# Kernel optimization log

Hardware: AMD Instinct MI355X
Metric: run time of the kernel (lower is better)

## Reference

```python
import jax, jax.numpy as jnp
import numpy as np

B, T, D = 4, 4096, 1024
EPS = 1e-5


def _layernorm(x, w):
    mu = jnp.mean(x, axis=-1, keepdims=True)
    var = jnp.var(x, axis=-1, keepdims=True)
    return (x - mu) * jax.lax.rsqrt(var + EPS) * w


def setup_inputs() -> dict:
    key = jax.random.key(0)
    k0, k1, k2, k3 = jax.random.split(key, 4)
    x = jax.random.normal(k0, (B, T, D), dtype=jnp.float32)
    lengths = jax.random.randint(k1, (B,), 1, T + 1, dtype=jnp.int32)
    ln1_w = jnp.ones((D,), dtype=jnp.float32)
    ln2_w = jnp.ones((D,), dtype=jnp.float32)
    Wfc = jax.random.normal(k2, (D, 4 * D), dtype=jnp.float32) * 0.02
    Wproj = jax.random.normal(k3, (4 * D, D), dtype=jnp.float32) * 0.02
    return {"x": x, "lengths": lengths, "ln1_w": ln1_w, "ln2_w": ln2_w,
            "Wfc": Wfc, "Wproj": Wproj}


def reference(x, lengths, ln1_w, ln2_w, Wfc, Wproj):
    b, t, d = x.shape
    # valid[b, i] = i < lengths[b]  (non-padded positions)
    valid = (jnp.arange(t)[None, :] < lengths[:, None]).astype(x.dtype)  # (B,T)

    # --- FusedQueryAtt: out[b,i] = h[b,i] + valid_i * sum_{j<=i} valid_j * gelu(h[b,j])
    h = _layernorm(x, ln1_w)
    g = jax.nn.gelu(h, approximate=False) * valid[:, :, None]  # (B,T,D)
    attn_out = h + valid[:, :, None] * jnp.cumsum(g, axis=1)
    x = x + attn_out  # residual around attn

    # --- MLP (bias=False, dropout=0 in eval)
    h2 = _layernorm(x, ln2_w)
    mlp_out = jax.nn.gelu(h2 @ Wfc, approximate=False) @ Wproj
    return x + mlp_out
```

## Files before the change

kernel.cpp:

```cpp
#include <hip/hip_runtime.h>
#include <hip/hip_bf16.h>
#include <math.h>

#define B_SZ 4
#define T_SZ 4096
#define D_SZ 1024
#define H_SZ 4096
#define CHUNK 16
#define NCHUNK (T_SZ / CHUNK)
#define LN_EPS 1e-5f

using frag8 = __attribute__((ext_vector_type(8))) short;
using f32x4 = __attribute__((ext_vector_type(4))) float;

__device__ __forceinline__ float gelu_exact(float x) {
  return 0.5f * x * (1.0f + erff(x * 0.70710678118654752f));
}

__device__ __forceinline__ float gelu_fast(float x) {
  float u2 = 1.5957691216057308f * (x + 0.044715f * x * x * x);
  float e = __expf(u2);
  return x - x * __builtin_amdgcn_rcpf(e + 1.0f);
}

__device__ __forceinline__ unsigned short f2bf(float f) {
  unsigned u = __float_as_uint(f);
  u += 0x7fffu + ((u >> 16) & 1u);
  return (unsigned short)(u >> 16);
}

__global__ __launch_bounds__(256) void ln_stats(
    const float* __restrict__ x, float2* __restrict__ stats) {
  __shared__ float red[8];
  int tid = threadIdx.x;
  size_t row = (size_t)blockIdx.x * D_SZ;
  float4 v = ((const float4*)(x + row))[tid];
  float s = v.x + v.y + v.z + v.w;
  float q = v.x * v.x + v.y * v.y + v.z * v.z + v.w * v.w;
#pragma unroll
  for (int o = 32; o > 0; o >>= 1) {
    s += __shfl_xor(s, o, 64);
    q += __shfl_xor(q, o, 64);
  }
  int w = tid >> 6;
  if ((tid & 63) == 0) { red[w * 2] = s; red[w * 2 + 1] = q; }
  __syncthreads();
  if (tid == 0) {
    s = red[0] + red[2] + red[4] + red[6];
    q = red[1] + red[3] + red[5] + red[7];
    float mu = s * (1.0f / D_SZ);
    float var = q * (1.0f / D_SZ) - mu * mu;
    float2 st; st.x = mu; st.y = rsqrtf(var + LN_EPS);
    stats[blockIdx.x] = st;
  }
}

__global__ __launch_bounds__(256) void attn_phase1(
    const float* __restrict__ x, const float2* __restrict__ stats,
    const int* __restrict__ lengths, const float* __restrict__ w1,
    float* __restrict__ partial, float* __restrict__ csum) {
  int b = blockIdx.x >> 8;
  int c = blockIdx.x & (NCHUNK - 1);
  int tid = threadIdx.x;
  int len = lengths[b];
  float4 w = ((const float4*)w1)[tid];
  float run0 = 0.f, run1 = 0.f, run2 = 0.f, run3 = 0.f;
#pragma unroll 4
  for (int i = 0; i < CHUNK; ++i) {
    int t = c * CHUNK + i;
    size_t row = ((size_t)b * T_SZ + t) * D_SZ;
    float4 v = ((const float4*)(x + row))[tid];
    float2 st = stats[b * T_SZ + t];
    bool valid = t < len;
    float hx = (v.x - st.x) * st.y * w.x, hy = (v.y - st.x) * st.y * w.y;
    float hz = (v.z - st.x) * st.y * w.z, hw = (v.w - st.x) * st.y * w.w;
    if (valid) {
      run0 += gelu_exact(hx); run1 += gelu_exact(hy);
      run2 += gelu_exact(hz); run3 += gelu_exact(hw);
    }
    float4 p;
    p.x = v.x + hx + (valid ? run0 : 0.f);
    p.y = v.y + hy + (valid ? run1 : 0.f);
    p.z = v.z + hz + (valid ? run2 : 0.f);
    p.w = v.w + hw + (valid ? run3 : 0.f);
    ((float4*)(partial + row))[tid] = p;
  }
  float4 cs; cs.x = run0; cs.y = run1; cs.z = run2; cs.w = run3;
  ((float4*)(csum + ((size_t)b * NCHUNK + c) * D_SZ))[tid] = cs;
}

__global__ __launch_bounds__(256) void chunk_scan(float* __restrict__ csum) {
  int idx = blockIdx.x * 256 + threadIdx.x;
  int b = idx >> 10;
  int d = idx & (D_SZ - 1);
  float* p = csum + (size_t)b * NCHUNK * D_SZ + d;
  float acc = 0.f;
#pragma unroll 8
  for (int c = 0; c < NCHUNK; ++c) {
    float t = p[(size_t)c * D_SZ];
    p[(size_t)c * D_SZ] = acc;
    acc += t;
  }
}

__global__ __launch_bounds__(256) void attn_phase2_ln2(
    float* __restrict__ xres, const float* __restrict__ csum,
    const int* __restrict__ lengths, const float* __restrict__ w2,
    unsigned short* __restrict__ h2) {
  __shared__ float red[8];
  int t = blockIdx.x & (T_SZ - 1);
  int b = blockIdx.x >> 12;
  int tid = threadIdx.x;
  bool valid = t < lengths[b];
  int c = t / CHUNK;
  size_t row = ((size_t)b * T_SZ + t) * D_SZ;
  float4 v = ((const float4*)(xres + row))[tid];
  if (valid) {
    float4 o = ((const float4*)(csum + ((size_t)b * NCHUNK + c) * D_SZ))[tid];
    v.x += o.x; v.y += o.y; v.z += o.z; v.w += o.w;
  }
  ((float4*)(xres + row))[tid] = v;
  float s = v.x + v.y + v.z + v.w;
  float q = v.x * v.x + v.y * v.y + v.z * v.z + v.w * v.w;
#pragma unroll
  for (int o = 32; o > 0; o >>= 1) {
    s += __shfl_xor(s, o, 64);
    q += __shfl_xor(q, o, 64);
  }
  int wv = tid >> 6;
  if ((tid & 63) == 0) { red[wv * 2] = s; red[wv * 2 + 1] = q; }
  __syncthreads();
  s = red[0] + red[2] + red[4] + red[6];
  q = red[1] + red[3] + red[5] + red[7];
  float mu = s * (1.0f / D_SZ);
  float var = q * (1.0f / D_SZ) - mu * mu;
  float rstd = rsqrtf(var + LN_EPS);
  float4 w = ((const float4*)w2)[tid];
  ushort4 hq;
  hq.x = f2bf((v.x - mu) * rstd * w.x);
  hq.y = f2bf((v.y - mu) * rstd * w.y);
  hq.z = f2bf((v.z - mu) * rstd * w.z);
  hq.w = f2bf((v.w - mu) * rstd * w.w);
  ((ushort4*)(h2 + row))[tid] = hq;
}

__global__ __launch_bounds__(256) void transpose_f32_to_bf16(
    const float* __restrict__ src, unsigned short* __restrict__ dst,
    int R, int C) {
  __shared__ float tile[32][33];
  int bx = blockIdx.x * 32;
  int by = blockIdx.y * 32;
  int tx = threadIdx.x & 31;
  int ty = threadIdx.x >> 5;
#pragma unroll
  for (int i = 0; i < 32; i += 8)
    tile[ty + i][tx] = src[(size_t)(by + ty + i) * C + bx + tx];
  __syncthreads();
#pragma unroll
  for (int i = 0; i < 32; i += 8)
    dst[(size_t)(bx + ty + i) * R + by + tx] = f2bf(tile[tx][ty + i]);
}

__device__ __forceinline__ void gld_lds16(const unsigned short* g,
                                          unsigned short* l) {
  __builtin_amdgcn_global_load_lds(
      (const __attribute__((address_space(1))) unsigned int*)g,
      (__attribute__((address_space(3))) unsigned int*)l, 16, 0, 0);
}

#define GT_TILE (256 * 64)

__device__ __forceinline__ void stageA(const unsigned short* A_blk, int K,
                                       unsigned short* as_buf, int h, int k0,
                                       int tid) {
#pragma unroll
  for (int j = 0; j < 2; ++j) {
    int R = j * 128 + h * 64 + (tid >> 3);
    int kc = ((tid & 7) * 8) ^ ((R & 7) << 3);
    gld_lds16(A_blk + (size_t)R * K + k0 + kc,
              as_buf + R * 64 + (tid & 7) * 8);
  }
}

__device__ __forceinline__ void stageB(const unsigned short* B_blk, int K,
                                       unsigned short* bs_buf, int h, int k0,
                                       int tid) {
  int lr = tid >> 3;
#pragma unroll
  for (int j = 0; j < 2; ++j) {
    int R = j * 128 + (lr >> 5) * 64 + h * 32 + (lr & 31);
    int kc = ((tid & 7) * 8) ^ ((R & 7) << 3);
    gld_lds16(B_blk + (size_t)R * K + k0 + kc,
              bs_buf + R * 64 + (tid & 7) * 8);
  }
}

template <int MH>
__device__ __forceinline__ void load_a(const unsigned short* As_c,
                                       frag8 (&af)[4][2], int wm, int r16,
                                       int quad) {
#pragma unroll
  for (int tm = 0; tm < 4; ++tm)
#pragma unroll
    for (int kk = 0; kk < 2; ++kk) {
      int r = wm * 128 + MH * 64 + tm * 16 + r16;
      int cb = (kk * 64 + quad * 16) ^ ((r16 & 7) << 4);
      af[tm][kk] = *(const frag8*)(As_c + r * 64 + (cb >> 1));
    }
}

template <int NH>
__device__ __forceinline__ void load_b(const unsigned short* Bs_c,
                                       frag8 (&bfr)[2][2][2], int wn, int r16,
                                       int quad) {
#pragma unroll
  for (int tn = 0; tn < 2; ++tn)
#pragma unroll
    for (int kk = 0; kk < 2; ++kk) {
      int r = wn * 64 + NH * 32 + tn * 16 + r16;
      int cb = (kk * 64 + quad * 16) ^ ((r16 & 7) << 4);
      bfr[NH][tn][kk] = *(const frag8*)(Bs_c + r * 64 + (cb >> 1));
    }
}

template <int MH, int NH>
__device__ __forceinline__ void mfma_q(f32x4 (&acc)[8][4],
                                       const frag8 (&af)[4][2],
                                       const frag8 (&bfr)[2][2][2]) {
#pragma unroll
  for (int kk = 0; kk < 2; ++kk)
#pragma unroll
    for (int tm = 0; tm < 4; ++tm)
#pragma unroll
      for (int tn = 0; tn < 2; ++tn)
        acc[MH * 4 + tm][NH * 2 + tn] =
            __builtin_amdgcn_mfma_f32_16x16x32_bf16(
                af[tm][kk], bfr[NH][tn][kk], acc[MH * 4 + tm][NH * 2 + tn],
                0, 0, 0);
}

#define GBAR()                          \
  do {                                  \
    asm volatile("" ::: "memory");      \
    __builtin_amdgcn_s_barrier();       \
    asm volatile("" ::: "memory");      \
  } while (0)

__global__ __launch_bounds__(512, 2) void gemm256_bt(
    const unsigned short* __restrict__ A, const unsigned short* __restrict__ Bt,
    int N, int K, int gx,
    const float* __restrict__ resid, float* __restrict__ outf,
    unsigned short* __restrict__ outb, int epi) {
  extern __shared__ unsigned short smem[];
  unsigned short* As = smem;
  unsigned short* Bs = smem + 2 * GT_TILE;

  int orig = blockIdx.x, nwg = gridDim.x;
  int wg = orig;
  if ((nwg & 7) == 0) wg = (orig & 7) * (nwg >> 3) + (orig >> 3);
  int bx = wg % gx, by = wg / gx;
  int bm = by * 256, bn = bx * 256;

  int tid = threadIdx.x;
  int lane = tid & 63, wave = tid >> 6;
  int wm = wave >> 2, wn = wave & 3;
  int quad = lane >> 4, r16 = lane & 15;

  const unsigned short* A_blk = A + (size_t)bm * K;
  const unsigned short* B_blk = Bt + (size_t)bn * K;
  int nt = K >> 6;

  f32x4 acc[8][4] = {};
  frag8 af[4][2];
  frag8 bfr[2][2][2];

  stageA(A_blk, K, As, 0, 0, tid);
  stageA(A_blk, K, As, 1, 0, tid);
  stageB(B_blk, K, Bs, 0, 0, tid);
  stageB(B_blk, K, Bs, 1, 0, tid);
  if (nt > 1) {
    stageA(A_blk, K, As + GT_TILE, 0, 64, tid);
    stageB(B_blk, K, Bs + GT_TILE, 0, 64, tid);
    stageB(B_blk, K, Bs + GT_TILE, 1, 64, tid);
    asm volatile("s_waitcnt vmcnt(6)" ::: "memory");
  } else {
    asm volatile("s_waitcnt vmcnt(0)" ::: "memory");
  }
  GBAR();

  for (int t = 0; t < nt; ++t) {
    unsigned short* As_c = As + (t & 1) * GT_TILE;
    unsigned short* Bs_c = Bs + (t & 1) * GT_TILE;
    unsigned short* As_n = As + ((t + 1) & 1) * GT_TILE;
    bool p1 = (t + 1 < nt), p2 = (t + 2 < nt);

    load_a<0>(As_c, af, wm, r16, quad);
    load_b<0>(Bs_c, bfr, wn, r16, quad);
    if (p1) stageA(A_blk, K, As_n, 1, (t + 1) * 64, tid);
    asm volatile("s_waitcnt lgkmcnt(8)" ::: "memory");
    GBAR();
    asm volatile("s_waitcnt lgkmcnt(0)" ::: "memory");
    __builtin_amdgcn_s_setprio(1);
    mfma_q<0, 0>(acc, af, bfr);
    __builtin_amdgcn_s_setprio(0);
    GBAR();

    load_b<1>(Bs_c, bfr, wn, r16, quad);
    if (p2) stageA(A_blk, K, As_c, 0, (t + 2) * 64, tid);
    GBAR();
    asm volatile("s_waitcnt lgkmcnt(0)" ::: "memory");
    __builtin_amdgcn_s_setprio(1);
    mfma_q<0, 1>(acc, af, bfr);
    __builtin_amdgcn_s_setprio(0);
    GBAR();

    load_a<1>(As_c, af, wm, r16, quad);
    if (p2) stageB(B_blk, K, Bs_c, 0, (t + 2) * 64, tid);
    GBAR();
    asm volatile("s_waitcnt lgkmcnt(0)" ::: "memory");
    __builtin_amdgcn_s_setprio(1);
    mfma_q<1, 1>(acc, af, bfr);
    __builtin_amdgcn_s_setprio(0);
    GBAR();

    if (p2) {
      stageB(B_blk, K, Bs_c, 1, (t + 2) * 64, tid);
      asm volatile("s_waitcnt vmcnt(6)" ::: "memory");
    } else {
      asm volatile("s_waitcnt vmcnt(0)" ::: "memory");
    }
    GBAR();
    __builtin_amdgcn_s_setprio(1);
    mfma_q<1, 0>(acc, af, bfr);
    __builtin_amdgcn_s_setprio(0);
    GBAR();
  }

  if (epi == 0) {
#pragma unroll
    for (int mf = 0; mf < 8; ++mf) {
#pragma unroll
      for (int nf = 0; nf < 4; ++nf) {
        int gm0 = bm + wm * 128 + mf * 16 + quad * 4;
        int gn = bn + wn * 64 + nf * 16 + r16;
#pragma unroll
        for (int r = 0; r < 4; ++r)
          outb[(size_t)(gm0 + r) * N + gn] = f2bf(gelu_fast(acc[mf][nf][r]));
      }
    }
  } else {
#pragma unroll
    for (int mf = 0; mf < 8; ++mf) {
#pragma unroll
      for (int nf = 0; nf < 4; ++nf) {
        int gm0 = bm + wm * 128 + mf * 16 + quad * 4;
        int gn = bn + wn * 64 + nf * 16 + r16;
#pragma unroll
        for (int r = 0; r < 4; ++r)
          outf[(size_t)(gm0 + r) * N + gn] =
              resid[(size_t)(gm0 + r) * N + gn] + acc[mf][nf][r];
      }
    }
  }
}

extern "C" void kernel_launch(void* const* d_in, const int* in_sizes, int n_in,
                              void* d_out, int out_size, void* d_ws,
                              size_t ws_size, hipStream_t stream) {
  const float* x = (const float*)d_in[0];
  const int* lengths = (const int*)d_in[1];
  const float* ln1_w = (const float*)d_in[2];
  const float* ln2_w = (const float*)d_in[3];
  const float* Wfc = (const float*)d_in[4];
  const float* Wproj = (const float*)d_in[5];
  float* out = (float*)d_out;

  static bool lds_cfg = false;
  if (!lds_cfg) {
    hipFuncSetAttribute((const void*)gemm256_bt,
                        hipFuncAttributeMaxDynamicSharedMemorySize, 131072);
    lds_cfg = true;
  }

  char* ws = (char*)d_ws;
  size_t off = 0;
  float2* stats = (float2*)(ws + off);
  off += (size_t)B_SZ * T_SZ * sizeof(float2);
  float* csum = (float*)(ws + off);
  off += (size_t)B_SZ * NCHUNK * D_SZ * sizeof(float);
  unsigned short* wfcb = (unsigned short*)(ws + off);
  off += (size_t)D_SZ * H_SZ * sizeof(unsigned short);
  unsigned short* wprojb = (unsigned short*)(ws + off);
  off += (size_t)H_SZ * D_SZ * sizeof(unsigned short);
  unsigned short* h2 = (unsigned short*)(ws + off);
  off += (size_t)B_SZ * T_SZ * D_SZ * sizeof(unsigned short);
  unsigned short* act = (unsigned short*)(ws + off);

  const int M = B_SZ * T_SZ;
  const size_t tileBytes = 256ull * H_SZ * sizeof(unsigned short);
  size_t avail = (ws_size > off) ? (ws_size - off) : 0;
  int sliceTiles = (int)(avail / tileBytes);
  if (sliceTiles < 1) sliceTiles = 1;
  int sliceM = sliceTiles * 256;
  if (sliceM > M) sliceM = M;

  ln_stats<<<B_SZ * T_SZ, 256, 0, stream>>>(x, stats);
  attn_phase1<<<B_SZ * NCHUNK, 256, 0, stream>>>(x, stats, lengths, ln1_w,
                                                 out, csum);
  chunk_scan<<<(B_SZ * D_SZ) / 256, 256, 0, stream>>>(csum);
  attn_phase2_ln2<<<B_SZ * T_SZ, 256, 0, stream>>>(out, csum, lengths, ln2_w, h2);
  transpose_f32_to_bf16<<<dim3(H_SZ / 32, D_SZ / 32), 256, 0, stream>>>(
      Wfc, wfcb, D_SZ, H_SZ);
  transpose_f32_to_bf16<<<dim3(D_SZ / 32, H_SZ / 32), 256, 0, stream>>>(
      Wproj, wprojb, H_SZ, D_SZ);

  for (int m0 = 0; m0 < M; m0 += sliceM) {
    int rows = (M - m0 < sliceM) ? (M - m0) : sliceM;
    int r1 = rows / 256;
    gemm256_bt<<<dim3((H_SZ / 256) * r1), 512, 131072, stream>>>(
        h2 + (size_t)m0 * D_SZ, wfcb, H_SZ, D_SZ, H_SZ / 256,
        nullptr, nullptr, act, 0);
    gemm256_bt<<<dim3((D_SZ / 256) * r1), 512, 131072, stream>>>(
        act, wprojb, D_SZ, H_SZ, D_SZ / 256,
        out + (size_t)m0 * D_SZ, out + (size_t)m0 * D_SZ, nullptr, 1);
  }
}
```

Before: 485.1 us.

## Double-buffer GEMM register fragments to overlap LDS reads with MFMA

Splits the A and B register fragments into two sets so the next quadrant's LDS loads are issued before the current quadrant's MFMAs run. The next tile's first fragments are prefetched inside the previous iteration. The explicit lgkmcnt waits are removed, which leaves the compiler to insert them. This is meant to hide LDS read latency behind matrix math. In exchange it uses more VGPRs and reorders the global stage waits (vmcnt 4), which risks spills at 512 threads with 2 blocks per CU, or subtle ordering hazards.

```diff
diff --git a/kernel.cpp b/kernel.cpp
--- a/kernel.cpp
+++ b/kernel.cpp
@@ -195,38 +195,36 @@
   }
 }
 
-template <int MH>
-__device__ __forceinline__ void load_a(const unsigned short* As_c,
-                                       frag8 (&af)[4][2], int wm, int r16,
-                                       int quad) {
+__device__ __forceinline__ void load_afrag(const unsigned short* base,
+                                           frag8 (&dst)[4][2], int mh, int wm,
+                                           int r16, int quad) {
 #pragma unroll
   for (int tm = 0; tm < 4; ++tm)
 #pragma unroll
     for (int kk = 0; kk < 2; ++kk) {
-      int r = wm * 128 + MH * 64 + tm * 16 + r16;
+      int r = wm * 128 + mh * 64 + tm * 16 + r16;
       int cb = (kk * 64 + quad * 16) ^ ((r16 & 7) << 4);
-      af[tm][kk] = *(const frag8*)(As_c + r * 64 + (cb >> 1));
-    }
-}
-
-template <int NH>
-__device__ __forceinline__ void load_b(const unsigned short* Bs_c,
-                                       frag8 (&bfr)[2][2][2], int wn, int r16,
-                                       int quad) {
+      dst[tm][kk] = *(const frag8*)(base + r * 64 + (cb >> 1));
+    }
+}
+
+__device__ __forceinline__ void load_bfrag(const unsigned short* base,
+                                           frag8 (&dst)[2][2], int nh, int wn,
+                                           int r16, int quad) {
 #pragma unroll
   for (int tn = 0; tn < 2; ++tn)
 #pragma unroll
     for (int kk = 0; kk < 2; ++kk) {
-      int r = wn * 64 + NH * 32 + tn * 16 + r16;
+      int r = wn * 64 + nh * 32 + tn * 16 + r16;
       int cb = (kk * 64 + quad * 16) ^ ((r16 & 7) << 4);
-      bfr[NH][tn][kk] = *(const frag8*)(Bs_c + r * 64 + (cb >> 1));
+      dst[tn][kk] = *(const frag8*)(base + r * 64 + (cb >> 1));
     }
 }
 
 template <int MH, int NH>
 __device__ __forceinline__ void mfma_q(f32x4 (&acc)[8][4],
-                                       const frag8 (&af)[4][2],
-                                       const frag8 (&bfr)[2][2][2]) {
+                                       const frag8 (&a)[4][2],
+                                       const frag8 (&b)[2][2]) {
 #pragma unroll
   for (int kk = 0; kk < 2; ++kk)
 #pragma unroll
@@ -235,8 +233,7 @@
       for (int tn = 0; tn < 2; ++tn)
         acc[MH * 4 + tm][NH * 2 + tn] =
             __builtin_amdgcn_mfma_f32_16x16x32_bf16(
-                af[tm][kk], bfr[NH][tn][kk], acc[MH * 4 + tm][NH * 2 + tn],
-                0, 0, 0);
+                a[tm][kk], b[tn][kk], acc[MH * 4 + tm][NH * 2 + tn], 0, 0, 0);
 }
 
 #define GBAR()                          \
@@ -271,8 +268,8 @@
   int nt = K >> 6;
 
   f32x4 acc[8][4] = {};
-  frag8 af[4][2];
-  frag8 bfr[2][2][2];
+  frag8 af0[4][2], af1[4][2];
+  frag8 b0[2][2], b1[2][2];
 
   stageA(A_blk, K, As, 0, 0, tid);
   stageA(A_blk, K, As, 1, 0, tid);
@@ -287,52 +284,51 @@
     asm volatile("s_waitcnt vmcnt(0)" ::: "memory");
   }
   GBAR();
+  load_afrag(As, af0, 0, wm, r16, quad);
+  load_bfrag(Bs, b0, 0, wn, r16, quad);
 
   for (int t = 0; t < nt; ++t) {
     unsigned short* As_c = As + (t & 1) * GT_TILE;
     unsigned short* Bs_c = Bs + (t & 1) * GT_TILE;
     unsigned short* As_n = As + ((t + 1) & 1) * GT_TILE;
+    unsigned short* Bs_n = Bs + ((t + 1) & 1) * GT_TILE;
     bool p1 = (t + 1 < nt), p2 = (t + 2 < nt);
 
-    load_a<0>(As_c, af, wm, r16, quad);
-    load_b<0>(Bs_c, bfr, wn, r16, quad);
+    load_bfrag(Bs_c, b1, 1, wn, r16, quad);
     if (p1) stageA(A_blk, K, As_n, 1, (t + 1) * 64, tid);
-    asm volatile("s_waitcnt lgkmcnt(8)" ::: "memory");
-    GBAR();
-    asm volatile("s_waitcnt lgkmcnt(0)" ::: "memory");
+    GBAR();
     __builtin_amdgcn_s_setprio(1);
-    mfma_q<0, 0>(acc, af, bfr);
+    mfma_q<0, 0>(acc, af0, b0);
     __builtin_amdgcn_s_setprio(0);
     GBAR();
 
-    load_b<1>(Bs_c, bfr, wn, r16, quad);
+    load_afrag(As_c, af1, 1, wm, r16, quad);
     if (p2) stageA(A_blk, K, As_c, 0, (t + 2) * 64, tid);
     GBAR();
-    asm volatile("s_waitcnt lgkmcnt(0)" ::: "memory");
     __builtin_amdgcn_s_setprio(1);
-    mfma_q<0, 1>(acc, af, bfr);
+    mfma_q<0, 1>(acc, af0, b1);
     __builtin_amdgcn_s_setprio(0);
     GBAR();
 
-    load_a<1>(As_c, af, wm, r16, quad);
-    if (p2) stageB(B_blk, K, Bs_c, 0, (t + 2) * 64, tid);
-    GBAR();
-    asm volatile("s_waitcnt lgkmcnt(0)" ::: "memory");
-    __builtin_amdgcn_s_setprio(1);
-    mfma_q<1, 1>(acc, af, bfr);
-    __builtin_amdgcn_s_setprio(0);
-    GBAR();
-
     if (p2) {
-      stageB(B_blk, K, Bs_c, 1, (t + 2) * 64, tid);
-      asm volatile("s_waitcnt vmcnt(6)" ::: "memory");
+      stageB(B_blk, K, Bs_c, 0, (t + 2) * 64, tid);
+      asm volatile("s_waitcnt vmcnt(4)" ::: "memory");
     } else {
       asm volatile("s_waitcnt vmcnt(0)" ::: "memory");
     }
     GBAR();
+    if (p1) load_afrag(As_n, af0, 0, wm, r16, quad);
     __builtin_amdgcn_s_setprio(1);
-    mfma_q<1, 0>(acc, af, bfr);
+    mfma_q<1, 1>(acc, af1, b1);
     __builtin_amdgcn_s_setprio(0);
+    GBAR();
+
+    if (p2) stageB(B_blk, K, Bs_c, 1, (t + 2) * 64, tid);
+    GBAR();
+    __builtin_amdgcn_s_setprio(1);
+    mfma_q<1, 0>(acc, af1, b0);
+    __builtin_amdgcn_s_setprio(0);
+    if (p1) load_bfrag(Bs_n, b0, 0, wn, r16, quad);
     GBAR();
   }
 
```

New measurement: 592.7 us. 22.2% more time.
